# Optimization experiments

Measured on AMD Instinct MI355X. Metric: run time of the kernel, lower is better.

Reference implementation:

```python
import jax, jax.numpy as jnp
import numpy as np

D_MODEL = 1024
H = 16
D_K = D_MODEL // H
NEG = -1e9


def setup_inputs() -> dict:
    key = jax.random.key(0)
    ks = jax.random.split(key, 13)
    B, S = 4, 2048
    q = jax.random.normal(ks[0], (B, S, D_MODEL), dtype=jnp.float32)
    k = jax.random.normal(ks[1], (B, S, D_MODEL), dtype=jnp.float32)
    v = jax.random.normal(ks[2], (B, S, D_MODEL), dtype=jnp.float32)
    mask = jax.random.randint(ks[3], (B, 1, S, S), 0, 2, dtype=jnp.int32)
    s = 1.0 / np.sqrt(D_MODEL)
    wq = jax.random.uniform(ks[4], (D_MODEL, D_MODEL), jnp.float32, -s, s)
    bq = jax.random.uniform(ks[5], (D_MODEL,), jnp.float32, -s, s)
    wk = jax.random.uniform(ks[6], (D_MODEL, D_MODEL), jnp.float32, -s, s)
    bk = jax.random.uniform(ks[7], (D_MODEL,), jnp.float32, -s, s)
    wv = jax.random.uniform(ks[8], (D_MODEL, D_MODEL), jnp.float32, -s, s)
    bv = jax.random.uniform(ks[9], (D_MODEL,), jnp.float32, -s, s)
    wo = jax.random.uniform(ks[10], (D_MODEL, D_MODEL), jnp.float32, -s, s)
    bo = jax.random.uniform(ks[11], (D_MODEL,), jnp.float32, -s, s)
    return {"q": q, "k": k, "v": v, "mask": mask,
            "wq": wq, "bq": bq, "wk": wk, "bk": bk,
            "wv": wv, "bv": bv, "wo": wo, "bo": bo}


def reference(q, k, v, mask, wq, bq, wk, bk, wv, bv, wo, bo):
    B, S, _ = q.shape
    # projections (torch Linear: x @ W.T + b)
    query = q @ wq.T + bq
    key_ = k @ wk.T + bk
    value = v @ wv.T + bv
    # [B, S, H, D_K] -> [B, H, S, D_K]
    query = query.reshape(B, S, H, D_K).transpose(0, 2, 1, 3)
    key_ = key_.reshape(B, S, H, D_K).transpose(0, 2, 1, 3)
    value = value.reshape(B, S, H, D_K).transpose(0, 2, 1, 3)
    scores = jnp.einsum('bhqd,bhkd->bhqk', query, key_) / jnp.sqrt(jnp.float32(D_K))
    scores = jnp.where(mask == 0, jnp.float32(NEG), scores)
    attn = jax.nn.softmax(scores, axis=-1)  # dropout p=0 -> identity
    x = jnp.einsum('bhqk,bhkd->bhqd', attn, value)
    x = x.transpose(0, 2, 1, 3).reshape(B, S, D_MODEL)
    return x @ wo.T + bo
```

## Files before the change

kernel.cpp:

```cpp
#include <hip/hip_runtime.h>
#include <stdint.h>
#include <stddef.h>


typedef unsigned short ushort_t;
typedef unsigned long long u64;
typedef __attribute__((ext_vector_type(8))) short short8;
typedef __attribute__((ext_vector_type(4))) float floatx4;
typedef __attribute__((ext_vector_type(4))) unsigned short ushort4v;

#define QSCALE (0.125f * 1.4426950408889634f)

__device__ __forceinline__ ushort_t f2bf(float f) {
    union { float ff; unsigned int i; } v; v.ff = f;
    unsigned int u = v.i;
    return (ushort_t)((u + 0x7fffu + ((u >> 16) & 1u)) >> 16);
}
__device__ __forceinline__ ushort_t f2bf_fast(float f) {
    union { float ff; unsigned int i; } v; v.ff = f;
    return (ushort_t)((v.i + 0x8000u) >> 16);
}
__device__ __forceinline__ float fexp2(float x) {
#if __has_builtin(__builtin_amdgcn_exp2f)
    return __builtin_amdgcn_exp2f(x);
#else
    return exp2f(x);
#endif
}

__device__ __forceinline__ void g2l16(const void* g, void* l) {
    __builtin_amdgcn_global_load_lds(
        (const __attribute__((address_space(1))) void*)(uintptr_t)g,
        (__attribute__((address_space(3))) void*)(uint32_t)(uintptr_t)l,
        16, 0, 0);
}

__global__ __launch_bounds__(256) void conv_f32_bf16(
    const float* __restrict__ in, ushort_t* __restrict__ out)
{
    const int i = blockIdx.x * 256 + threadIdx.x;
    const float4 v = ((const float4*)in)[i];
    ushort4v o;
    o.x = f2bf(v.x); o.y = f2bf(v.y); o.z = f2bf(v.z); o.w = f2bf(v.w);
    ((ushort4v*)out)[i] = o;
}

__global__ __launch_bounds__(256) void mask_pack(
    const int* __restrict__ m, u64* __restrict__ out)
{
    const int gid = blockIdx.x * 256 + threadIdx.x;
    const u64 bits = __ballot(m[gid] != 0);
    if ((threadIdx.x & 63) == 0) out[gid >> 6] = bits;
}

template <int MODE>
__global__ __launch_bounds__(256, 2) void gemm_bt(
    const ushort_t* __restrict__ A, const ushort_t* __restrict__ W,
    const float* __restrict__ bias, void* __restrict__ Cout, float scale)
{
    constexpr int N = 1024, K = 1024;
    __shared__ alignas(16) ushort_t As[128 * 32];
    __shared__ alignas(16) ushort_t Bs[128 * 32];

    const int tid  = threadIdx.x;
    const int lane = tid & 63;
    const int w    = tid >> 6;
    const int quad = lane >> 4;
    const int l16  = lane & 15;
    const int wm = w >> 1, wn = w & 1;
    const int bm = blockIdx.y * 128, bn = blockIdx.x * 128;

    const int ar0 = tid >> 2,         acs0 = ((tid & 3) ^ (ar0 & 3)) * 8;
    const int ar1 = (tid + 256) >> 2, acs1 = ((tid & 3) ^ (ar1 & 3)) * 8;

    const ushort_t* Ast0 = A + (size_t)(bm + ar0) * K + acs0;
    const ushort_t* Ast1 = A + (size_t)(bm + ar1) * K + acs1;
    const ushort_t* Wst0 = W + (size_t)(bn + ar0) * K + acs0;
    const ushort_t* Wst1 = W + (size_t)(bn + ar1) * K + acs1;

    const int ksw = (quad ^ (l16 & 3)) * 8;
    int asoff[4], bsoff[4];
#pragma unroll
    for (int i = 0; i < 4; i++) {
        asoff[i] = (wm * 64 + i * 16 + l16) * 32 + ksw;
        bsoff[i] = (wn * 64 + i * 16 + l16) * 32 + ksw;
    }

    floatx4 acc[4][4] = {};

    for (int kt = 0; kt < K; kt += 32) {
        __syncthreads();
        g2l16(Ast0 + kt, &As[tid * 8]);
        g2l16(Ast1 + kt, &As[(tid + 256) * 8]);
        g2l16(Wst0 + kt, &Bs[tid * 8]);
        g2l16(Wst1 + kt, &Bs[(tid + 256) * 8]);
        __syncthreads();

        short8 af[4], bf[4];
#pragma unroll
        for (int i = 0; i < 4; i++) af[i] = *(const short8*)&As[asoff[i]];
#pragma unroll
        for (int i = 0; i < 4; i++) bf[i] = *(const short8*)&Bs[bsoff[i]];
#pragma unroll
        for (int mi = 0; mi < 4; mi++)
#pragma unroll
            for (int ni = 0; ni < 4; ni++)
                acc[mi][ni] = __builtin_amdgcn_mfma_f32_16x16x32_bf16(
                    af[mi], bf[ni], acc[mi][ni], 0, 0, 0);
    }

#pragma unroll
    for (int ni = 0; ni < 4; ni++) {
        const int n = bn + wn * 64 + ni * 16 + l16;
        const float bv = bias[n];
#pragma unroll
        for (int mi = 0; mi < 4; mi++) {
            const int mbase = bm + wm * 64 + mi * 16 + quad * 4;
            if (MODE == 2) {
                const int b_ = mbase >> 11, s0 = mbase & 2047;
                const int h = n >> 6, d = n & 63;
                ushort4v pk;
#pragma unroll
                for (int r = 0; r < 4; r++)
                    pk[r] = f2bf((acc[mi][ni][r] + bv) * scale);
                *(ushort4v*)&((ushort_t*)Cout)[
                    (((size_t)(b_ * 16 + h)) * 64 + d) * 2048 + s0] = pk;
            } else {
#pragma unroll
                for (int r = 0; r < 4; r++) {
                    const int m = mbase + r;
                    const float of = (acc[mi][ni][r] + bv) * scale;
                    if (MODE == 0) {
                        ((float*)Cout)[(size_t)m * N + n] = of;
                    } else {
                        const int b_ = m >> 11, s = m & 2047;
                        const int h = n >> 6, d = n & 63;
                        ((ushort_t*)Cout)[(((size_t)(b_ * 16 + h)) * 2048 + s) * 64 + d]
                            = f2bf(of);
                    }
                }
            }
        }
    }
}

__global__ __launch_bounds__(256, 3) void attn(
    const ushort_t* __restrict__ Q,
    const ushort_t* __restrict__ Kk,
    const ushort_t* __restrict__ Vt,
    const u64* __restrict__ mb,
    ushort_t* __restrict__ X)
{
    constexpr int S = 2048;
    __shared__ alignas(16) ushort_t Ks[64 * 64];
    __shared__ alignas(16) ushort_t Vs[64 * 64];
    __shared__ alignas(16) ushort_t Ps[4][16 * 64];

    const int tid  = threadIdx.x;
    const int lane = tid & 63;
    const int w    = tid >> 6;
    const int quad = lane >> 4;
    const int l16  = lane & 15;
    const int bh = blockIdx.y;
    const int b  = bh >> 4, h = bh & 15;
    const int qbase = blockIdx.x * 64 + w * 16;

    const int r0 = tid >> 3,         cs0 = ((tid & 7) ^ (r0 & 7)) * 8;
    const int r1 = (tid + 256) >> 3, cs1 = ((tid & 7) ^ (r1 & 7)) * 8;

    const ushort_t* Kst0 = &Kk[((size_t)bh * S + r0) * 64 + cs0];
    const ushort_t* Kst1 = &Kk[((size_t)bh * S + r1) * 64 + cs1];
    const ushort_t* Vst0 = &Vt[((size_t)bh * 64 + r0) * S + cs0];
    const ushort_t* Vst1 = &Vt[((size_t)bh * 64 + r1) * S + cs1];

    const int swz = l16 & 7;
    int kvoff[2][4], pfoff[2], pwoff[4][4];
#pragma unroll
    for (int ks = 0; ks < 2; ks++) {
        pfoff[ks] = l16 * 64 + (((ks * 4 + quad) ^ swz) * 8);
#pragma unroll
        for (int ni = 0; ni < 4; ni++)
            kvoff[ks][ni] = (ni * 16 + l16) * 64 + (((ks * 4 + quad) ^ swz) * 8);
    }
#pragma unroll
    for (int ni = 0; ni < 4; ni++)
#pragma unroll
        for (int r = 0; r < 4; r++) {
            const int row = quad * 4 + r, col = ni * 16 + l16;
            pwoff[ni][r] = row * 64 + (((col >> 3) ^ (row & 7)) * 8) + (col & 7);
        }
    ushort_t* Psw = &Ps[w][0];

    short8 qf[2];
#pragma unroll
    for (int ks = 0; ks < 2; ks++)
        qf[ks] = *(const short8*)&Q[((size_t)bh * S + qbase + l16) * 64 + ks * 32 + quad * 8];

    short8 onesv;
#pragma unroll
    for (int i = 0; i < 8; i++) onesv[i] = (short)0x3F80;

    const u64* mrow = mb + ((size_t)b * S + qbase + quad * 4) * 32;

    floatx4 o[4] = {};
    floatx4 lf = {};

    for (int kt = 0; kt < 32; kt++) {
        __syncthreads();
        g2l16(Kst0 + kt * 4096, &Ks[tid * 8]);
        g2l16(Kst1 + kt * 4096, &Ks[(tid + 256) * 8]);
        g2l16(Vst0 + kt * 64,   &Vs[tid * 8]);
        g2l16(Vst1 + kt * 64,   &Vs[(tid + 256) * 8]);
        __syncthreads();

        floatx4 s[4] = {};
#pragma unroll
        for (int ks = 0; ks < 2; ks++)
#pragma unroll
            for (int ni = 0; ni < 4; ni++)
                s[ni] = __builtin_amdgcn_mfma_f32_16x16x32_bf16(
                    qf[ks], *(const short8*)&Ks[kvoff[ks][ni]], s[ni], 0, 0, 0);

#pragma unroll
        for (int r = 0; r < 4; r++) {
            const u64 msh = mrow[r * 32 + kt] >> l16;
#pragma unroll
            for (int ni = 0; ni < 4; ni++) {
                const bool keep = (msh >> (ni * 16)) & 1ull;
                s[ni][r] = keep ? fexp2(s[ni][r]) : 0.f;
            }
        }

#pragma unroll
        for (int ni = 0; ni < 4; ni++)
#pragma unroll
            for (int r = 0; r < 4; r++)
                Psw[pwoff[ni][r]] = f2bf_fast(s[ni][r]);

#pragma unroll
        for (int ks = 0; ks < 2; ks++) {
            const short8 pf = *(const short8*)&Psw[pfoff[ks]];
            lf = __builtin_amdgcn_mfma_f32_16x16x32_bf16(pf, onesv, lf, 0, 0, 0);
#pragma unroll
            for (int ni = 0; ni < 4; ni++)
                o[ni] = __builtin_amdgcn_mfma_f32_16x16x32_bf16(
                    pf, *(const short8*)&Vs[kvoff[ks][ni]], o[ni], 0, 0, 0);
        }
    }

    float inv[4];
#pragma unroll
    for (int r = 0; r < 4; r++) inv[r] = 1.0f / lf[r];
#pragma unroll
    for (int ni = 0; ni < 4; ni++)
#pragma unroll
        for (int r = 0; r < 4; r++) {
            const int qr = qbase + quad * 4 + r;
            const int d  = ni * 16 + l16;
            X[((size_t)b * S + qr) * 1024 + h * 64 + d] = f2bf(o[ni][r] * inv[r]);
        }
}

extern "C" void kernel_launch(void* const* d_in, const int* in_sizes, int n_in,
                              void* d_out, int out_size, void* d_ws, size_t ws_size,
                              hipStream_t stream) {
    const float* q    = (const float*)d_in[0];
    const float* k    = (const float*)d_in[1];
    const float* v    = (const float*)d_in[2];
    const int*   mask = (const int*)d_in[3];
    const float* wq   = (const float*)d_in[4];
    const float* bq   = (const float*)d_in[5];
    const float* wk   = (const float*)d_in[6];
    const float* bk   = (const float*)d_in[7];
    const float* wv   = (const float*)d_in[8];
    const float* bv   = (const float*)d_in[9];
    const float* wo   = (const float*)d_in[10];
    const float* bo   = (const float*)d_in[11];

    const size_t MB = 1024 * 1024;
    uint8_t* ws = (uint8_t*)d_ws;
    ushort_t* Abuf  = (ushort_t*)(ws);
    ushort_t* Wbuf  = (ushort_t*)(ws + 16 * MB);
    u64*      mbits = (u64*)(ws + 16 * MB);
    ushort_t* Qp    = (ushort_t*)(ws + 18 * MB);
    ushort_t* Kp    = (ushort_t*)(ws + 34 * MB);
    ushort_t* Vtp   = (ushort_t*)(ws + 50 * MB);

    dim3 blk(256);
    dim3 gg(8, 64);
    const int gA = (4 * 2048 * 1024) / 1024;
    const int gW = (1024 * 1024) / 1024;
    const int gM = (4 * 2048 * 2048) / 256;

    conv_f32_bf16<<<gA, blk, 0, stream>>>(q, Abuf);
    conv_f32_bf16<<<gW, blk, 0, stream>>>(wq, Wbuf);
    gemm_bt<1><<<gg, blk, 0, stream>>>(Abuf, Wbuf, bq, Qp, QSCALE);

    conv_f32_bf16<<<gA, blk, 0, stream>>>(k, Abuf);
    conv_f32_bf16<<<gW, blk, 0, stream>>>(wk, Wbuf);
    gemm_bt<1><<<gg, blk, 0, stream>>>(Abuf, Wbuf, bk, Kp, 1.0f);

    conv_f32_bf16<<<gA, blk, 0, stream>>>(v, Abuf);
    conv_f32_bf16<<<gW, blk, 0, stream>>>(wv, Wbuf);
    gemm_bt<2><<<gg, blk, 0, stream>>>(Abuf, Wbuf, bv, Vtp, 1.0f);

    mask_pack<<<gM, blk, 0, stream>>>(mask, mbits);
    attn<<<dim3(32, 64), blk, 0, stream>>>(Qp, Kp, Vtp, mbits, Abuf);

    conv_f32_bf16<<<gW, blk, 0, stream>>>(wo, Wbuf);
    gemm_bt<0><<<gg, blk, 0, stream>>>(Abuf, Wbuf, bo, d_out, 1.0f);
}
```

Measured before the change: 490.1 us.

## Fuse fp32-to-bf16 activation conversion into GEMMs and transpose attention MFMA layout

The projection GEMMs now read fp32 activations directly and convert them to bf16 in registers before storing to LDS, which removes three standalone conversion kernels and their round-trip through global memory. The four weight conversions are merged into one launch. The attention kernel swaps MFMA operand order so each lane owns one query row, which lets it use a single mask word per tile, packed 64-bit P stores and vectorized output stores. Grid axes are swapped in both the GEMMs and attention. The fp32 A loads go through registers and lose the async global-to-LDS path, which may expose more load latency in the GEMMs.

```diff
diff --git a/kernel.cpp b/kernel.cpp
--- a/kernel.cpp
+++ b/kernel.cpp
@@ -8,6 +8,7 @@
 typedef __attribute__((ext_vector_type(8))) short short8;
 typedef __attribute__((ext_vector_type(4))) float floatx4;
 typedef __attribute__((ext_vector_type(4))) unsigned short ushort4v;
+typedef __attribute__((ext_vector_type(4))) unsigned int uint4v;
 
 #define QSCALE (0.125f * 1.4426950408889634f)
 
@@ -16,9 +17,9 @@
     unsigned int u = v.i;
     return (ushort_t)((u + 0x7fffu + ((u >> 16) & 1u)) >> 16);
 }
-__device__ __forceinline__ ushort_t f2bf_fast(float f) {
-    union { float ff; unsigned int i; } v; v.ff = f;
-    return (ushort_t)((v.i + 0x8000u) >> 16);
+__device__ __forceinline__ unsigned int pack2bf(float a, float b) {
+    union { float f; unsigned int i; } ua, ub; ua.f = a; ub.f = b;
+    return ((ua.i + 0x8000u) >> 16) | ((ub.i + 0x8000u) & 0xffff0000u);
 }
 __device__ __forceinline__ float fexp2(float x) {
 #if __has_builtin(__builtin_amdgcn_exp2f)
@@ -27,7 +28,6 @@
     return exp2f(x);
 #endif
 }
-
 __device__ __forceinline__ void g2l16(const void* g, void* l) {
     __builtin_amdgcn_global_load_lds(
         (const __attribute__((address_space(1))) void*)(uintptr_t)g,
@@ -35,14 +35,18 @@
         16, 0, 0);
 }
 
-__global__ __launch_bounds__(256) void conv_f32_bf16(
-    const float* __restrict__ in, ushort_t* __restrict__ out)
+__global__ __launch_bounds__(256) void conv_w4(
+    const float* __restrict__ w0, const float* __restrict__ w1,
+    const float* __restrict__ w2, const float* __restrict__ w3,
+    ushort_t* __restrict__ out)
 {
+    const int seg = blockIdx.y;
+    const float* src = (seg == 0) ? w0 : (seg == 1) ? w1 : (seg == 2) ? w2 : w3;
     const int i = blockIdx.x * 256 + threadIdx.x;
-    const float4 v = ((const float4*)in)[i];
+    const float4 v = ((const float4*)src)[i];
     ushort4v o;
     o.x = f2bf(v.x); o.y = f2bf(v.y); o.z = f2bf(v.z); o.w = f2bf(v.w);
-    ((ushort4v*)out)[i] = o;
+    ((ushort4v*)(out + (size_t)seg * 1024 * 1024))[i] = o;
 }
 
 __global__ __launch_bounds__(256) void mask_pack(
@@ -53,9 +57,9 @@
     if ((threadIdx.x & 63) == 0) out[gid >> 6] = bits;
 }
 
-template <int MODE>
+template <int MODE, int AF32>
 __global__ __launch_bounds__(256, 2) void gemm_bt(
-    const ushort_t* __restrict__ A, const ushort_t* __restrict__ W,
+    const void* __restrict__ Ain, const ushort_t* __restrict__ W,
     const float* __restrict__ bias, void* __restrict__ Cout, float scale)
 {
     constexpr int N = 1024, K = 1024;
@@ -68,15 +72,21 @@
     const int quad = lane >> 4;
     const int l16  = lane & 15;
     const int wm = w >> 1, wn = w & 1;
-    const int bm = blockIdx.y * 128, bn = blockIdx.x * 128;
+    const int bm = blockIdx.x * 128, bn = blockIdx.y * 128;
 
     const int ar0 = tid >> 2,         acs0 = ((tid & 3) ^ (ar0 & 3)) * 8;
     const int ar1 = (tid + 256) >> 2, acs1 = ((tid & 3) ^ (ar1 & 3)) * 8;
 
-    const ushort_t* Ast0 = A + (size_t)(bm + ar0) * K + acs0;
-    const ushort_t* Ast1 = A + (size_t)(bm + ar1) * K + acs1;
     const ushort_t* Wst0 = W + (size_t)(bn + ar0) * K + acs0;
     const ushort_t* Wst1 = W + (size_t)(bn + ar1) * K + acs1;
+
+    const int arow = tid >> 1, ahalf = tid & 1;
+    const float* Af = (const float*)Ain + (size_t)(bm + arow) * K + ahalf * 16;
+    const int ac0 = ((2 * ahalf + 0) ^ (arow & 3)) * 8;
+    const int ac1 = ((2 * ahalf + 1) ^ (arow & 3)) * 8;
+
+    const ushort_t* Ast0 = (const ushort_t*)Ain + (size_t)(bm + ar0) * K + acs0;
+    const ushort_t* Ast1 = (const ushort_t*)Ain + (size_t)(bm + ar1) * K + acs1;
 
     const int ksw = (quad ^ (l16 & 3)) * 8;
     int asoff[4], bsoff[4];
@@ -89,9 +99,24 @@
     floatx4 acc[4][4] = {};
 
     for (int kt = 0; kt < K; kt += 32) {
+        float4 f0, f1, f2, f3;
+        if (AF32) {
+            const float4* ap = (const float4*)(Af + kt);
+            f0 = ap[0]; f1 = ap[1]; f2 = ap[2]; f3 = ap[3];
+        }
         __syncthreads();
-        g2l16(Ast0 + kt, &As[tid * 8]);
-        g2l16(Ast1 + kt, &As[(tid + 256) * 8]);
+        if (AF32) {
+            uint4v c0, c1;
+            c0.x = pack2bf(f0.x, f0.y); c0.y = pack2bf(f0.z, f0.w);
+            c0.z = pack2bf(f1.x, f1.y); c0.w = pack2bf(f1.z, f1.w);
+            c1.x = pack2bf(f2.x, f2.y); c1.y = pack2bf(f2.z, f2.w);
+            c1.z = pack2bf(f3.x, f3.y); c1.w = pack2bf(f3.z, f3.w);
+            *(uint4v*)&As[arow * 32 + ac0] = c0;
+            *(uint4v*)&As[arow * 32 + ac1] = c1;
+        } else {
+            g2l16(Ast0 + kt, &As[tid * 8]);
+            g2l16(Ast1 + kt, &As[(tid + 256) * 8]);
+        }
         g2l16(Wst0 + kt, &Bs[tid * 8]);
         g2l16(Wst1 + kt, &Bs[(tid + 256) * 8]);
         __syncthreads();
@@ -161,9 +186,10 @@
     const int w    = tid >> 6;
     const int quad = lane >> 4;
     const int l16  = lane & 15;
-    const int bh = blockIdx.y;
+    const int bh = blockIdx.x;
     const int b  = bh >> 4, h = bh & 15;
-    const int qbase = blockIdx.x * 64 + w * 16;
+    const int qbase = blockIdx.y * 64 + w * 16;
+    const int qlane = qbase + l16;
 
     const int r0 = tid >> 3,         cs0 = ((tid & 7) ^ (r0 & 7)) * 8;
     const int r1 = (tid + 256) >> 3, cs1 = ((tid & 7) ^ (r1 & 7)) * 8;
@@ -174,7 +200,7 @@
     const ushort_t* Vst1 = &Vt[((size_t)bh * 64 + r1) * S + cs1];
 
     const int swz = l16 & 7;
-    int kvoff[2][4], pfoff[2], pwoff[4][4];
+    int kvoff[2][4], pfoff[2], pwoff[4];
 #pragma unroll
     for (int ks = 0; ks < 2; ks++) {
         pfoff[ks] = l16 * 64 + (((ks * 4 + quad) ^ swz) * 8);
@@ -184,23 +210,19 @@
     }
 #pragma unroll
     for (int ni = 0; ni < 4; ni++)
-#pragma unroll
-        for (int r = 0; r < 4; r++) {
-            const int row = quad * 4 + r, col = ni * 16 + l16;
-            pwoff[ni][r] = row * 64 + (((col >> 3) ^ (row & 7)) * 8) + (col & 7);
-        }
+        pwoff[ni] = l16 * 64 + (((ni * 2 + (quad >> 1)) ^ swz) * 8) + (quad & 1) * 4;
     ushort_t* Psw = &Ps[w][0];
 
     short8 qf[2];
 #pragma unroll
     for (int ks = 0; ks < 2; ks++)
-        qf[ks] = *(const short8*)&Q[((size_t)bh * S + qbase + l16) * 64 + ks * 32 + quad * 8];
+        qf[ks] = *(const short8*)&Q[((size_t)bh * S + qlane) * 64 + ks * 32 + quad * 8];
 
     short8 onesv;
 #pragma unroll
     for (int i = 0; i < 8; i++) onesv[i] = (short)0x3F80;
 
-    const u64* mrow = mb + ((size_t)b * S + qbase + quad * 4) * 32;
+    const u64* mrow = mb + ((size_t)b * S + qlane) * 32;
 
     floatx4 o[4] = {};
     floatx4 lf = {};
@@ -219,46 +241,44 @@
 #pragma unroll
             for (int ni = 0; ni < 4; ni++)
                 s[ni] = __builtin_amdgcn_mfma_f32_16x16x32_bf16(
-                    qf[ks], *(const short8*)&Ks[kvoff[ks][ni]], s[ni], 0, 0, 0);
-
-#pragma unroll
-        for (int r = 0; r < 4; r++) {
-            const u64 msh = mrow[r * 32 + kt] >> l16;
-#pragma unroll
-            for (int ni = 0; ni < 4; ni++) {
-                const bool keep = (msh >> (ni * 16)) & 1ull;
-                s[ni][r] = keep ? fexp2(s[ni][r]) : 0.f;
-            }
-        }
-
-#pragma unroll
-        for (int ni = 0; ni < 4; ni++)
+                    *(const short8*)&Ks[kvoff[ks][ni]], qf[ks], s[ni], 0, 0, 0);
+
+        const u64 mw = mrow[kt];
+#pragma unroll
+        for (int ni = 0; ni < 4; ni++) {
+            const unsigned int t = (unsigned int)(mw >> (ni * 16 + quad * 4));
 #pragma unroll
             for (int r = 0; r < 4; r++)
-                Psw[pwoff[ni][r]] = f2bf_fast(s[ni][r]);
+                s[ni][r] = (t & (1u << r)) ? fexp2(s[ni][r]) : 0.f;
+        }
+
+#pragma unroll
+        for (int ni = 0; ni < 4; ni++) {
+            unsigned int lo = pack2bf(s[ni][0], s[ni][1]);
+            unsigned int hi = pack2bf(s[ni][2], s[ni][3]);
+            unsigned long long dv = ((unsigned long long)hi << 32) | lo;
+            *(unsigned long long*)&Psw[pwoff[ni]] = dv;
+        }
 
 #pragma unroll
         for (int ks = 0; ks < 2; ks++) {
             const short8 pf = *(const short8*)&Psw[pfoff[ks]];
-            lf = __builtin_amdgcn_mfma_f32_16x16x32_bf16(pf, onesv, lf, 0, 0, 0);
+            lf = __builtin_amdgcn_mfma_f32_16x16x32_bf16(onesv, pf, lf, 0, 0, 0);
 #pragma unroll
             for (int ni = 0; ni < 4; ni++)
                 o[ni] = __builtin_amdgcn_mfma_f32_16x16x32_bf16(
-                    pf, *(const short8*)&Vs[kvoff[ks][ni]], o[ni], 0, 0, 0);
-        }
-    }
-
-    float inv[4];
-#pragma unroll
-    for (int r = 0; r < 4; r++) inv[r] = 1.0f / lf[r];
-#pragma unroll
-    for (int ni = 0; ni < 4; ni++)
-#pragma unroll
-        for (int r = 0; r < 4; r++) {
-            const int qr = qbase + quad * 4 + r;
-            const int d  = ni * 16 + l16;
-            X[((size_t)b * S + qr) * 1024 + h * 64 + d] = f2bf(o[ni][r] * inv[r]);
-        }
+                    *(const short8*)&Vs[kvoff[ks][ni]], pf, o[ni], 0, 0, 0);
+        }
+    }
+
+    const float inv = 1.0f / lf[0];
+#pragma unroll
+    for (int ni = 0; ni < 4; ni++) {
+        ushort4v pk;
+#pragma unroll
+        for (int r = 0; r < 4; r++) pk[r] = f2bf(o[ni][r] * inv);
+        *(ushort4v*)&X[((size_t)b * S + qlane) * 1024 + h * 64 + ni * 16 + quad * 4] = pk;
+    }
 }
 
 extern "C" void kernel_launch(void* const* d_in, const int* in_sizes, int n_in,
@@ -279,34 +299,26 @@
 
     const size_t MB = 1024 * 1024;
     uint8_t* ws = (uint8_t*)d_ws;
-    ushort_t* Abuf  = (ushort_t*)(ws);
-    ushort_t* Wbuf  = (ushort_t*)(ws + 16 * MB);
-    u64*      mbits = (u64*)(ws + 16 * MB);
-    ushort_t* Qp    = (ushort_t*)(ws + 18 * MB);
-    ushort_t* Kp    = (ushort_t*)(ws + 34 * MB);
-    ushort_t* Vtp   = (ushort_t*)(ws + 50 * MB);
+    ushort_t* Wb   = (ushort_t*)(ws);
+    u64*      mbits= (u64*)(ws + 8 * MB);
+    ushort_t* Qp   = (ushort_t*)(ws + 10 * MB);
+    ushort_t* Kp   = (ushort_t*)(ws + 26 * MB);
+    ushort_t* Vtp  = (ushort_t*)(ws + 42 * MB);
+    ushort_t* Xp   = (ushort_t*)(ws + 58 * MB);
 
     dim3 blk(256);
-    dim3 gg(8, 64);
-    const int gA = (4 * 2048 * 1024) / 1024;
+    dim3 gg(64, 8);
     const int gW = (1024 * 1024) / 1024;
     const int gM = (4 * 2048 * 2048) / 256;
 
-    conv_f32_bf16<<<gA, blk, 0, stream>>>(q, Abuf);
-    conv_f32_bf16<<<gW, blk, 0, stream>>>(wq, Wbuf);
-    gemm_bt<1><<<gg, blk, 0, stream>>>(Abuf, Wbuf, bq, Qp, QSCALE);
-
-    conv_f32_bf16<<<gA, blk, 0, stream>>>(k, Abuf);
-    conv_f32_bf16<<<gW, blk, 0, stream>>>(wk, Wbuf);
-    gemm_bt<1><<<gg, blk, 0, stream>>>(Abuf, Wbuf, bk, Kp, 1.0f);
-
-    conv_f32_bf16<<<gA, blk, 0, stream>>>(v, Abuf);
-    conv_f32_bf16<<<gW, blk, 0, stream>>>(wv, Wbuf);
-    gemm_bt<2><<<gg, blk, 0, stream>>>(Abuf, Wbuf, bv, Vtp, 1.0f);
-
+    conv_w4<<<dim3(gW, 4), blk, 0, stream>>>(wq, wk, wv, wo, Wb);
     mask_pack<<<gM, blk, 0, stream>>>(mask, mbits);
-    attn<<<dim3(32, 64), blk, 0, stream>>>(Qp, Kp, Vtp, mbits, Abuf);
-
-    conv_f32_bf16<<<gW, blk, 0, stream>>>(wo, Wbuf);
-    gemm_bt<0><<<gg, blk, 0, stream>>>(Abuf, Wbuf, bo, d_out, 1.0f);
-}
+
+    gemm_bt<1, 1><<<gg, blk, 0, stream>>>(q, Wb,                bq, Qp,  QSCALE);
+    gemm_bt<1, 1><<<gg, blk, 0, stream>>>(k, Wb + 1 * MB,       bk, Kp,  1.0f);
+    gemm_bt<2, 1><<<gg, blk, 0, stream>>>(v, Wb + 2 * MB,       bv, Vtp, 1.0f);
+
+    attn<<<dim3(64, 32), blk, 0, stream>>>(Qp, Kp, Vtp, mbits, Xp);
+
+    gemm_bt<0, 0><<<gg, blk, 0, stream>>>(Xp, Wb + 3 * MB,      bo, d_out, 1.0f);
+}
```

After: 475.0 us. 1.03x faster.
